# Optimization experiments

Measured on AMD Instinct MI355X. Metric: run time of the kernel, lower is better.

Reference implementation:

```python
import jax, jax.numpy as jnp
import numpy as np
from jax import lax

SIGMOID_THRESH = 0.05  # hard-coded in get_local_max_coords
KERNEL = 3             # default kernel_size


def setup_inputs() -> dict:
    key = jax.random.key(0)
    # [B, num_kps, H, W] heatmap logits from the DeepLab head
    heatmaps = jax.random.normal(key, (16, 17, 384, 384), dtype=jnp.float32)
    return {"heatmaps": heatmaps}


def reference(heatmaps):
    """CenterNet-style local-max peak extraction.

    Faithful to Heatmaps.get_local_max_coords: a pixel is a peak iff it equals
    the 3x3 max-pool of the logits AND sigmoid(logit) > 0.05. Instead of the
    data-dependent torch.nonzero + Python grouping loops (which just reshuffle
    the same information into ragged per-image/per-type lists), we return the
    dense, fixed-shape peak-score map: sigmoid(logit) at peak locations, 0
    elsewhere. The [B, K, H, W] layout already encodes the per-image (axis 0)
    and per-keypoint-type (axis 1) grouping of the original nested loops.
    """
    # 3x3 max-pool, stride 1, SAME padding (pad = kernel // 2)
    max_hm = lax.reduce_window(
        heatmaps,
        -jnp.inf,
        lax.max,
        window_dimensions=(1, 1, KERNEL, KERNEL),
        window_strides=(1, 1, 1, 1),
        padding="SAME",
    )
    prob = jax.nn.sigmoid(heatmaps)
    peak_mask = (max_hm == heatmaps) & (prob > SIGMOID_THRESH)
    return jnp.where(peak_mask, prob, jnp.zeros((), dtype=heatmaps.dtype))
```

## Files before the change

kernel.cpp:

```cpp
#include <hip/hip_runtime.h>
#include <math.h>

#define HH 384
#define WW 384
#define W4 96
#define YO8 48
#define NIMG 272
#define IMG_STRIDE (HH * WW)
#define TOTAL_THR (NIMG * YO8 * W4)

typedef float f4_t __attribute__((ext_vector_type(4)));

__device__ __forceinline__ float fast_sigmoid(float v) {
    return __fdividef(1.0f, 1.0f + __expf(-v));
}

__device__ __forceinline__ float max3f(float a, float b, float c) {
    return fmaxf(fmaxf(a, b), c);
}

__global__ __launch_bounds__(256) void
heatmap_peaks_kernel(const float* __restrict__ in, float* __restrict__ out) {
    int vi   = blockIdx.x * 256 + threadIdx.x;
    int lane = threadIdx.x & 63;

    int x4   = vi % W4;
    int rest = vi / W4;
    int yo   = rest % YO8;
    int bk   = rest / YO8;
    int y0   = yo * 8;

    const float NEG = -INFINITY;
    const float* base = in + (size_t)bk * IMG_STRIDE + x4 * 4;

    float4 R[10];
#pragma unroll
    for (int j = 0; j < 10; ++j) {
        int yy = y0 - 1 + j;
        bool valid = (yy >= 0) && (yy < HH);
        int yc = yy < 0 ? 0 : (yy >= HH ? HH - 1 : yy);
        float4 v = *(const float4*)(base + (size_t)yc * WW);
        if (!valid) v = make_float4(NEG, NEG, NEG, NEG);
        R[j] = v;
    }

    float cl[10], cr[10];
#pragma unroll
    for (int j = 0; j < 10; ++j) { cl[j] = NEG; cr[j] = NEG; }

    bool has_l = (x4 > 0) && (lane == 0);
    bool has_r = (x4 < W4 - 1) && (lane == 63);
    if (has_l) {
#pragma unroll
        for (int j = 0; j < 10; ++j) {
            int yy = y0 - 1 + j;
            if (yy >= 0 && yy < HH) cl[j] = base[(size_t)yy * WW - 1];
        }
    }
    if (has_r) {
#pragma unroll
        for (int j = 0; j < 10; ++j) {
            int yy = y0 - 1 + j;
            if (yy >= 0 && yy < HH) cr[j] = base[(size_t)yy * WW + 4];
        }
    }

    float* ob = out + (size_t)bk * IMG_STRIDE + (size_t)y0 * WW + x4 * 4;

#pragma unroll
    for (int r = 0; r < 8; ++r) {
        float4 A = R[r], B = R[r + 1], C = R[r + 2];
        float4 vm;
        vm.x = max3f(A.x, B.x, C.x);
        vm.y = max3f(A.y, B.y, C.y);
        vm.z = max3f(A.z, B.z, C.z);
        vm.w = max3f(A.w, B.w, C.w);

        float lvm = __shfl_up(vm.w, 1);
        float rvm = __shfl_down(vm.x, 1);
        if (x4 == 0)            lvm = NEG;
        else if (lane == 0)     lvm = max3f(cl[r], cl[r + 1], cl[r + 2]);
        if (x4 == W4 - 1)       rvm = NEG;
        else if (lane == 63)    rvm = max3f(cr[r], cr[r + 1], cr[r + 2]);

        float4 m;
        m.x = max3f(lvm,  vm.x, vm.y);
        m.y = max3f(vm.x, vm.y, vm.z);
        m.z = max3f(vm.y, vm.z, vm.w);
        m.w = max3f(vm.z, vm.w, rvm);

        float p;
        f4_t o;
        p = fast_sigmoid(B.x); o.x = (m.x == B.x && p > 0.05f) ? p : 0.0f;
        p = fast_sigmoid(B.y); o.y = (m.y == B.y && p > 0.05f) ? p : 0.0f;
        p = fast_sigmoid(B.z); o.z = (m.z == B.z && p > 0.05f) ? p : 0.0f;
        p = fast_sigmoid(B.w); o.w = (m.w == B.w && p > 0.05f) ? p : 0.0f;

        __builtin_nontemporal_store(o, (f4_t*)(ob + (size_t)r * WW));
    }
}

extern "C" void kernel_launch(void* const* d_in, const int* in_sizes, int n_in,
                              void* d_out, int out_size, void* d_ws, size_t ws_size,
                              hipStream_t stream) {
    const float* in = (const float*)d_in[0];
    float* out = (float*)d_out;
    int blocks = TOTAL_THR / 256;
    heatmap_peaks_kernel<<<blocks, 256, 0, stream>>>(in, out);
}
```

Before: 273.3 us.

## Stage 66x66 halo tiles in LDS for 3x3 max-pool peak detection

Replaces per-thread 8-row column strips with float4 loads and wave shuffles by 64x64 output tiles per block. Each block loads a 66x66 haloed tile into shared memory, and each thread then computes a 4x4 output patch from LDS. This cuts halo re-read traffic and removes shuffle and edge-lane special cases. In exchange it uses scalar global loads with integer division, adds an LDS round trip and a block barrier, and uses more shared memory per block.

```diff
diff --git a/kernel.cpp b/kernel.cpp
--- a/kernel.cpp
+++ b/kernel.cpp
@@ -3,99 +3,99 @@
 
 #define HH 384
 #define WW 384
-#define W4 96
-#define YO8 48
+#define TW 64
+#define TH 64
+#define TX 6
+#define TY 6
 #define NIMG 272
 #define IMG_STRIDE (HH * WW)
-#define TOTAL_THR (NIMG * YO8 * W4)
+#define LDS_W 67
+#define NELEM (66 * 66)
+#define NLOAD 18
 
 typedef float f4_t __attribute__((ext_vector_type(4)));
 
+__device__ __forceinline__ float max3f(float a, float b, float c) {
+    return fmaxf(fmaxf(a, b), c);
+}
 __device__ __forceinline__ float fast_sigmoid(float v) {
     return __fdividef(1.0f, 1.0f + __expf(-v));
 }
 
-__device__ __forceinline__ float max3f(float a, float b, float c) {
-    return fmaxf(fmaxf(a, b), c);
-}
-
 __global__ __launch_bounds__(256) void
 heatmap_peaks_kernel(const float* __restrict__ in, float* __restrict__ out) {
-    int vi   = blockIdx.x * 256 + threadIdx.x;
-    int lane = threadIdx.x & 63;
+    __shared__ float S[66 * LDS_W];
 
-    int x4   = vi % W4;
-    int rest = vi / W4;
-    int yo   = rest % YO8;
-    int bk   = rest / YO8;
-    int y0   = yo * 8;
+    int tid = threadIdx.x;
+    int bid = blockIdx.x;
+    int txt = bid % TX;
+    int tmp = bid / TX;
+    int tyt = tmp % TY;
+    int img = tmp / TY;
+    int x0 = txt * TW;
+    int y0 = tyt * TH;
 
+    const float* ib = in + (size_t)img * IMG_STRIDE;
     const float NEG = -INFINITY;
-    const float* base = in + (size_t)bk * IMG_STRIDE + x4 * 4;
 
-    float4 R[10];
+    float va[NLOAD];
+    bool  ok[NLOAD];
+    int   le[NLOAD];
 #pragma unroll
-    for (int j = 0; j < 10; ++j) {
-        int yy = y0 - 1 + j;
-        bool valid = (yy >= 0) && (yy < HH);
-        int yc = yy < 0 ? 0 : (yy >= HH ? HH - 1 : yy);
-        float4 v = *(const float4*)(base + (size_t)yc * WW);
-        if (!valid) v = make_float4(NEG, NEG, NEG, NEG);
-        R[j] = v;
+    for (int k = 0; k < NLOAD; ++k) {
+        int e  = tid + k * 256;
+        int ly = e / 66;
+        int lx = e - ly * 66;
+        int gx = x0 - 1 + lx;
+        int gy = y0 - 1 + ly;
+        bool valid = (e < NELEM) && ((unsigned)gx < (unsigned)WW)
+                                 && ((unsigned)gy < (unsigned)HH);
+        int cx = valid ? gx : 0;
+        int cy = valid ? gy : 0;
+        va[k] = ib[cy * WW + cx];
+        ok[k] = valid;
+        le[k] = ly * LDS_W + lx;
     }
+#pragma unroll
+    for (int k = 0; k < NLOAD; ++k) {
+        int e = tid + k * 256;
+        if (e < NELEM) S[le[k]] = ok[k] ? va[k] : NEG;
+    }
+    __syncthreads();
 
-    float cl[10], cr[10];
+    int ctx = tid & 15;
+    int cty = tid >> 4;
+    int rb  = cty * 4;
+    int cb  = ctx * 4;
+
+    float vals[6][6];
 #pragma unroll
-    for (int j = 0; j < 10; ++j) { cl[j] = NEG; cr[j] = NEG; }
+    for (int c = 0; c < 6; ++c)
+#pragma unroll
+        for (int r = 0; r < 6; ++r)
+            vals[c][r] = S[(rb + r) * LDS_W + cb + c];
 
-    bool has_l = (x4 > 0) && (lane == 0);
-    bool has_r = (x4 < W4 - 1) && (lane == 63);
-    if (has_l) {
+    float vm[6][4];
 #pragma unroll
-        for (int j = 0; j < 10; ++j) {
-            int yy = y0 - 1 + j;
-            if (yy >= 0 && yy < HH) cl[j] = base[(size_t)yy * WW - 1];
-        }
-    }
-    if (has_r) {
+    for (int c = 0; c < 6; ++c)
 #pragma unroll
-        for (int j = 0; j < 10; ++j) {
-            int yy = y0 - 1 + j;
-            if (yy >= 0 && yy < HH) cr[j] = base[(size_t)yy * WW + 4];
-        }
-    }
+        for (int r = 0; r < 4; ++r)
+            vm[c][r] = max3f(vals[c][r], vals[c][r + 1], vals[c][r + 2]);
 
-    float* ob = out + (size_t)bk * IMG_STRIDE + (size_t)y0 * WW + x4 * 4;
-
+    float* ob = out + (size_t)img * IMG_STRIDE
+                    + (size_t)(y0 + rb) * WW + x0 + cb;
 #pragma unroll
-    for (int r = 0; r < 8; ++r) {
-        float4 A = R[r], B = R[r + 1], C = R[r + 2];
-        float4 vm;
-        vm.x = max3f(A.x, B.x, C.x);
-        vm.y = max3f(A.y, B.y, C.y);
-        vm.z = max3f(A.z, B.z, C.z);
-        vm.w = max3f(A.w, B.w, C.w);
-
-        float lvm = __shfl_up(vm.w, 1);
-        float rvm = __shfl_down(vm.x, 1);
-        if (x4 == 0)            lvm = NEG;
-        else if (lane == 0)     lvm = max3f(cl[r], cl[r + 1], cl[r + 2]);
-        if (x4 == W4 - 1)       rvm = NEG;
-        else if (lane == 63)    rvm = max3f(cr[r], cr[r + 1], cr[r + 2]);
-
-        float4 m;
-        m.x = max3f(lvm,  vm.x, vm.y);
-        m.y = max3f(vm.x, vm.y, vm.z);
-        m.z = max3f(vm.y, vm.z, vm.w);
-        m.w = max3f(vm.z, vm.w, rvm);
-
-        float p;
+    for (int r = 0; r < 4; ++r) {
         f4_t o;
-        p = fast_sigmoid(B.x); o.x = (m.x == B.x && p > 0.05f) ? p : 0.0f;
-        p = fast_sigmoid(B.y); o.y = (m.y == B.y && p > 0.05f) ? p : 0.0f;
-        p = fast_sigmoid(B.z); o.z = (m.z == B.z && p > 0.05f) ? p : 0.0f;
-        p = fast_sigmoid(B.w); o.w = (m.w == B.w && p > 0.05f) ? p : 0.0f;
-
+        float p, m, v;
+        m = max3f(vm[0][r], vm[1][r], vm[2][r]); v = vals[1][r + 1];
+        p = fast_sigmoid(v); o.x = (m == v && p > 0.05f) ? p : 0.0f;
+        m = max3f(vm[1][r], vm[2][r], vm[3][r]); v = vals[2][r + 1];
+        p = fast_sigmoid(v); o.y = (m == v && p > 0.05f) ? p : 0.0f;
+        m = max3f(vm[2][r], vm[3][r], vm[4][r]); v = vals[3][r + 1];
+        p = fast_sigmoid(v); o.z = (m == v && p > 0.05f) ? p : 0.0f;
+        m = max3f(vm[3][r], vm[4][r], vm[5][r]); v = vals[4][r + 1];
+        p = fast_sigmoid(v); o.w = (m == v && p > 0.05f) ? p : 0.0f;
         __builtin_nontemporal_store(o, (f4_t*)(ob + (size_t)r * WW));
     }
 }
@@ -105,6 +105,6 @@
                               hipStream_t stream) {
     const float* in = (const float*)d_in[0];
     float* out = (float*)d_out;
-    int blocks = TOTAL_THR / 256;
+    int blocks = TX * TY * NIMG;
     heatmap_peaks_kernel<<<blocks, 256, 0, stream>>>(in, out);
 }
```

Result: faster. 260.8 us (-4.6%).
